# Kernel optimization log

Hardware: AMD Instinct MI355X
Metric: run time of the kernel (lower is better)

## Reference

```python
import jax, jax.numpy as jnp
import numpy as np

C_CODE, F_OUT, K_TOP, M_GRP, GROUPS, STRIDE, KSZ = 64, 256, 4, 8, 8, 4, 4
B, W, H = 4, 64, 64


def setup_inputs() -> dict:
    key = jax.random.key(0)
    k1, k2, k3, k4, k5 = jax.random.split(key, 5)
    shape = (B, K_TOP, M_GRP, W, H)
    ind_pos = jax.random.randint(k1, shape, 0, C_CODE, dtype=jnp.int32)
    ind_neg = jax.random.randint(k2, shape, 0, C_CODE, dtype=jnp.int32)
    val_pos = jax.random.normal(k3, shape, dtype=jnp.float32)
    val_neg = jax.random.normal(k4, shape, dtype=jnp.float32)
    # torch conv_transpose2d weight layout: [Cin, Cout/groups, kh, kw]
    weight = jax.random.normal(k5, (C_CODE * M_GRP, F_OUT // GROUPS, KSZ, KSZ), dtype=jnp.float32) * 0.05
    return {"ind_pos": ind_pos, "ind_neg": ind_neg, "val_pos": val_pos, "val_neg": val_neg, "weight": weight}


def _deindex_and_deconv(ind_pos, ind_neg, val_pos, val_neg, weight):
    b, k, m, w, h = ind_pos.shape
    c = C_CODE
    # offset each m-group's indices into the flattened c*m channel axis
    offs = (c * jnp.arange(m, dtype=jnp.int32)).reshape(1, 1, m, 1, 1)
    ip = (ind_pos + offs).reshape(b, k * m, w, h)
    iN = (ind_neg + offs).reshape(b, k * m, w, h)
    vp = val_pos.reshape(b, k * m, w, h)
    vn = val_neg.reshape(b, k * m, w, h)
    bb = jnp.arange(b).reshape(b, 1, 1, 1)
    ww = jnp.arange(w).reshape(1, 1, w, 1)
    hh = jnp.arange(h).reshape(1, 1, 1, h)
    out = jnp.zeros((b, c * m, w, h), dtype=vp.dtype)
    out = out.at[bb, ip, ww, hh].set(vp)  # scatter pos values along channel dim
    out = out.at[bb, iN, ww, hh].set(vn)  # neg scatter second (overwrites ties, like torch)
    # conv_transpose2d(stride=STRIDE, padding=0, groups=GROUPS) as dilated conv:
    # rearrange torch weight [Cin, Cout/g, kh, kw] -> OIHW [Cout, Cin/g, kh, kw], flip spatial
    cin, cog, kh, kw = weight.shape
    g = GROUPS
    rhs = weight.reshape(g, cin // g, cog, kh, kw).transpose(0, 2, 1, 3, 4).reshape(g * cog, cin // g, kh, kw)
    rhs = rhs[:, :, ::-1, ::-1]
    y = jax.lax.conv_general_dilated(
        out, rhs,
        window_strides=(1, 1),
        padding=[(kh - 1, kh - 1), (kw - 1, kw - 1)],
        lhs_dilation=(STRIDE, STRIDE),
        dimension_numbers=("NCHW", "OIHW", "NCHW"),
        feature_group_count=g,
    )
    return y


def reference(ind_pos, ind_neg, val_pos, val_neg, weight):
    return _deindex_and_deconv(ind_pos, ind_neg, val_pos, val_neg, weight)
```

## Files before the change

kernel.cpp:

```cpp
#include <hip/hip_runtime.h>


__global__ __launch_bounds__(256) void convdeidx_kernel(
    const int* __restrict__ ind_pos, const int* __restrict__ ind_neg,
    const float* __restrict__ val_pos, const float* __restrict__ val_neg,
    const float* __restrict__ weight, float* __restrict__ out)
{
    __shared__ float4 swt[2048];
    __shared__ __align__(16) int2 spair[64 * 10];

    const int bi  = blockIdx.x;
    const int i   = bi & 3;
    const int w   = (bi >> 2) & 63;
    const int m   = (bi >> 8) & 7;
    const int b   = bi >> 11;
    const int tid = threadIdx.x;

    {
        const int k = tid >> 6;
        const int h = tid & 63;
        const int idx = (((b * 4 + k) * 8 + m) * 64 + w) * 64 + h;
        spair[h * 10 + k]     = make_int2(ind_pos[idx], __float_as_int(val_pos[idx]));
        spair[h * 10 + 4 + k] = make_int2(ind_neg[idx], __float_as_int(val_neg[idx]));
    }
    {
        const float4* wsrc = (const float4*)weight;
        #pragma unroll
        for (int r = 0; r < 8; ++r) {
            const int l = r * 256 + tid;
            swt[l] = wsrc[(size_t)(2048 * m + l) * 4 + i];
        }
    }
    __syncthreads();

    if (tid < 64) {
        int c[8];
        #pragma unroll
        for (int p = 0; p < 8; ++p) c[p] = spair[tid * 10 + p].x;
        #pragma unroll
        for (int p = 0; p < 7; ++p) {
            bool dead = false;
            #pragma unroll
            for (int q = p + 1; q < 8; ++q) dead |= (c[q] == c[p]);
            if (dead) spair[tid * 10 + p].y = 0;
        }
    }
    __syncthreads();

    const int ocg  = tid & 31;
    const int hsub = tid >> 5;
    float* yrow = out + ((size_t)((b * 256 + m * 32 + ocg) * 256 + (w * 4 + i)) << 8);

    #pragma unroll
    for (int hc = 0; hc < 8; ++hc) {
        const int h = hc * 8 + hsub;
        const int4* pp = (const int4*)(spair + h * 10);
        float4 acc = make_float4(0.f, 0.f, 0.f, 0.f);
        #pragma unroll
        for (int pq = 0; pq < 4; ++pq) {
            const int4 two = pp[pq];
            const float  v0 = __int_as_float(two.y);
            const float  v1 = __int_as_float(two.w);
            const float4 w0 = swt[(two.x << 5) | ocg];
            const float4 w1 = swt[(two.z << 5) | ocg];
            acc.x += v0 * w0.x + v1 * w1.x;
            acc.y += v0 * w0.y + v1 * w1.y;
            acc.z += v0 * w0.z + v1 * w1.z;
            acc.w += v0 * w0.w + v1 * w1.w;
        }
        *reinterpret_cast<float4*>(yrow + 4 * h) = acc;
    }
}

extern "C" void kernel_launch(void* const* d_in, const int* in_sizes, int n_in,
                              void* d_out, int out_size, void* d_ws, size_t ws_size,
                              hipStream_t stream) {
    const int*   ind_pos = (const int*)  d_in[0];
    const int*   ind_neg = (const int*)  d_in[1];
    const float* val_pos = (const float*)d_in[2];
    const float* val_neg = (const float*)d_in[3];
    const float* weight  = (const float*)d_in[4];
    float*       y       = (float*)d_out;

    hipLaunchKernelGGL(convdeidx_kernel, dim3(8192), dim3(256), 0, stream,
                       ind_pos, ind_neg, val_pos, val_neg, weight, y);
}
```

Baseline: 334.0 us.

## Recast sparse deindex-deconv as dense bf16 MFMA GEMM with pre-transposed weights

Replaces the per-pair gather-FMA loop with a dense one-hot matrix built in shared memory and multiplied by bf16 weights using 16x16x32 MFMA instructions. A separate prologue kernel transposes the weights and converts them to bf16 in the workspace. One block now covers all four stride phases of a row, and output is written with nontemporal stores. The sparse activations are also rounded to bf16, which lowers precision, and a second launch is added.

```diff
diff --git a/kernel.cpp b/kernel.cpp
--- a/kernel.cpp
+++ b/kernel.cpp
@@ -1,74 +1,137 @@
 #include <hip/hip_runtime.h>
 
 
-__global__ __launch_bounds__(256) void convdeidx_kernel(
+typedef float f32x4  __attribute__((ext_vector_type(4)));
+typedef short bf16x8 __attribute__((ext_vector_type(8)));
+
+__device__ __forceinline__ unsigned short f32_to_bf16_rne(float f) {
+    unsigned int u = __float_as_uint(f);
+    return (unsigned short)((u + 0x7FFFu + ((u >> 16) & 1u)) >> 16);
+}
+
+__global__ __launch_bounds__(256) void wt_transpose_kernel(
+    const float* __restrict__ weight, unsigned short* __restrict__ ws)
+{
+    __shared__ unsigned short stile[64 * 72];
+    const int m    = blockIdx.x >> 3;
+    const int pblk = blockIdx.x & 7;
+    const int t    = threadIdx.x;
+    const int p    = t & 63;
+    const int chi  = t >> 6;
+    #pragma unroll
+    for (int r = 0; r < 16; ++r) {
+        const int c = chi * 16 + r;
+        const float v = weight[(size_t)(64 * m + c) * 512 + pblk * 64 + p];
+        stile[p * 72 + c] = f32_to_bf16_rne(v);
+    }
+    __syncthreads();
+    uint4* dst4 = (uint4*)(ws + (size_t)(m * 512 + pblk * 64) * 64);
+    #pragma unroll
+    for (int pass = 0; pass < 2; ++pass) {
+        const int g = pass * 256 + t;
+        const uint4 v = *(const uint4*)(stile + (g >> 3) * 72 + (g & 7) * 8);
+        dst4[g] = v;
+    }
+}
+
+__global__ __launch_bounds__(256) void convdeidx_mfma_kernel(
     const int* __restrict__ ind_pos, const int* __restrict__ ind_neg,
     const float* __restrict__ val_pos, const float* __restrict__ val_neg,
-    const float* __restrict__ weight, float* __restrict__ out)
+    const unsigned short* __restrict__ ws, float* __restrict__ out)
 {
-    __shared__ float4 swt[2048];
-    __shared__ __align__(16) int2 spair[64 * 10];
+    __shared__ unsigned short sA[256 * 72];
+    __shared__ unsigned short sX[64 * 72];
+    __shared__ int2 spair[64 * 10];
+
 
     const int bi  = blockIdx.x;
-    const int i   = bi & 3;
-    const int w   = (bi >> 2) & 63;
-    const int m   = (bi >> 8) & 7;
-    const int b   = bi >> 11;
+    const int w   = bi & 63;
+    const int m   = (bi >> 6) & 7;
+    const int b   = bi >> 9;
     const int tid = threadIdx.x;
+    const int wid = tid >> 6, lane = tid & 63;
+    const int q   = lane >> 4, ln = lane & 15;
 
     {
-        const int k = tid >> 6;
-        const int h = tid & 63;
+        const int k = tid >> 6, h = tid & 63;
         const int idx = (((b * 4 + k) * 8 + m) * 64 + w) * 64 + h;
         spair[h * 10 + k]     = make_int2(ind_pos[idx], __float_as_int(val_pos[idx]));
         spair[h * 10 + 4 + k] = make_int2(ind_neg[idx], __float_as_int(val_neg[idx]));
     }
     {
-        const float4* wsrc = (const float4*)weight;
+        uint4* x4 = (uint4*)sX;
+        const uint4 z = make_uint4(0u, 0u, 0u, 0u);
+        x4[tid] = z;
+        x4[tid + 256] = z;
+        if (tid < 64) x4[tid + 512] = z;
+    }
+    const uint4* wsrc4 = (const uint4*)(ws + (size_t)m * 512 * 64);
+    #pragma unroll
+    for (int r = 0; r < 8; ++r) {
+        const int g = r * 256 + tid;
+        const uint4 v = wsrc4[g];
+        *(uint4*)(sA + (g >> 3) * 72 + (g & 7) * 8) = v;
+    }
+    __syncthreads();
+
+    if (tid < 64) {
+        const int h = tid;
         #pragma unroll
-        for (int r = 0; r < 8; ++r) {
-            const int l = r * 256 + tid;
-            swt[l] = wsrc[(size_t)(2048 * m + l) * 4 + i];
+        for (int p = 0; p < 8; ++p) {
+            const int2 pr = spair[h * 10 + p];
+            sX[h * 72 + pr.x] = f32_to_bf16_rne(__int_as_float(pr.y));
         }
     }
     __syncthreads();
 
-    if (tid < 64) {
-        int c[8];
-        #pragma unroll
-        for (int p = 0; p < 8; ++p) c[p] = spair[tid * 10 + p].x;
-        #pragma unroll
-        for (int p = 0; p < 7; ++p) {
-            bool dead = false;
-            #pragma unroll
-            for (int q = p + 1; q < 8; ++q) dead |= (c[q] == c[p]);
-            if (dead) spair[tid * 10 + p].y = 0;
-        }
-    }
-    __syncthreads();
-
-    const int ocg  = tid & 31;
-    const int hsub = tid >> 5;
-    float* yrow = out + ((size_t)((b * 256 + m * 32 + ocg) * 256 + (w * 4 + i)) << 8);
+    f32x4* outv = (f32x4*)out;
 
     #pragma unroll
-    for (int hc = 0; hc < 8; ++hc) {
-        const int h = hc * 8 + hsub;
-        const int4* pp = (const int4*)(spair + h * 10);
-        float4 acc = make_float4(0.f, 0.f, 0.f, 0.f);
+    for (int chunk = 0; chunk < 2; ++chunk) {
+        if (chunk == 1) {
+            __syncthreads();
+            #pragma unroll
+            for (int r = 0; r < 8; ++r) {
+                const int g = r * 256 + tid;
+                const uint4 v = wsrc4[2048 + g];
+                *(uint4*)(sA + (g >> 3) * 72 + (g & 7) * 8) = v;
+            }
+            __syncthreads();
+        }
+
+        f32x4 acc[4][4];
         #pragma unroll
-        for (int pq = 0; pq < 4; ++pq) {
-            const int4 two = pp[pq];
-            const float  v0 = __int_as_float(two.y);
-            const float  v1 = __int_as_float(two.w);
-            const float4 w0 = swt[(two.x << 5) | ocg];
-            const float4 w1 = swt[(two.z << 5) | ocg];
-            acc.x += v0 * w0.x + v1 * w1.x;
-            acc.y += v0 * w0.y + v1 * w1.y;
-            acc.z += v0 * w0.z + v1 * w1.z;
-            acc.w += v0 * w0.w + v1 * w1.w;
+        for (int mt = 0; mt < 4; ++mt)
+            #pragma unroll
+            for (int nt = 0; nt < 4; ++nt)
+                acc[mt][nt] = (f32x4){0.f, 0.f, 0.f, 0.f};
+
+        #pragma unroll
+        for (int kt = 0; kt < 2; ++kt) {
+            bf16x8 afr[4], bfr[4];
+            #pragma unroll
+            for (int mt = 0; mt < 4; ++mt)
+                afr[mt] = *(const bf16x8*)(sA + (wid * 64 + mt * 16 + ln) * 72 + (kt * 4 + q) * 8);
+            #pragma unroll
+            for (int nt = 0; nt < 4; ++nt)
+                bfr[nt] = *(const bf16x8*)(sX + (nt * 16 + ln) * 72 + (kt * 4 + q) * 8);
+            #pragma unroll
+            for (int mt = 0; mt < 4; ++mt)
+                #pragma unroll
+                for (int nt = 0; nt < 4; ++nt)
+                    acc[mt][nt] = __builtin_amdgcn_mfma_f32_16x16x32_bf16(
+                        afr[mt], bfr[nt], acc[mt][nt], 0, 0, 0);
         }
-        *reinterpret_cast<float4*>(yrow + 4 * h) = acc;
+
+        const int ocg0 = chunk * 16 + wid * 4;
+        #pragma unroll
+        for (int mt = 0; mt < 4; ++mt) {
+            const size_t rowbase =
+                ((size_t)(b * 256 + m * 32 + ocg0 + mt) * 256 + (w * 4 + q)) * 64;
+            #pragma unroll
+            for (int nt = 0; nt < 4; ++nt)
+                __builtin_nontemporal_store(acc[mt][nt], outv + rowbase + nt * 16 + ln);
+        }
     }
 }
 
@@ -81,7 +144,9 @@
     const float* val_neg = (const float*)d_in[3];
     const float* weight  = (const float*)d_in[4];
     float*       y       = (float*)d_out;
+    unsigned short* ws   = (unsigned short*)d_ws;
 
-    hipLaunchKernelGGL(convdeidx_kernel, dim3(8192), dim3(256), 0, stream,
-                       ind_pos, ind_neg, val_pos, val_neg, weight, y);
+    hipLaunchKernelGGL(wt_transpose_kernel, dim3(64), dim3(256), 0, stream, weight, ws);
+    hipLaunchKernelGGL(convdeidx_mfma_kernel, dim3(2048), dim3(256), 0, stream,
+                       ind_pos, ind_neg, val_pos, val_neg, ws, y);
 }
```

New measurement: 282.3 us. 15.5% less time.
